# Kernel optimization log

Measured on AMD Instinct MI355X. Metric: run time of the kernel, lower is better.

## Reference

```python
import jax, jax.numpy as jnp
import numpy as np

L = 512
Z_DIM = 128
C = 128
EPS = 1e-5


def _ln(x, g, b):
    m = jnp.mean(x, axis=-1, keepdims=True)
    v = jnp.var(x, axis=-1, keepdims=True)
    return (x - m) * jax.lax.rsqrt(v + EPS) * g + b


def setup_inputs() -> dict:
    key = jax.random.key(0)
    ks = jax.random.split(key, 12)
    s_z = 1.0 / np.sqrt(Z_DIM)
    s_c = 1.0 / np.sqrt(C)
    return {
        "z": jax.random.normal(ks[0], (L, L, Z_DIM), dtype=jnp.float32),
        "norm_g": jnp.ones((Z_DIM,), jnp.float32),
        "norm_b": jnp.zeros((Z_DIM,), jnp.float32),
        "a_w": jax.random.normal(ks[1], (C, Z_DIM), jnp.float32) * s_z,
        "a_b": jnp.zeros((C,), jnp.float32),
        "ag_w": jax.random.normal(ks[2], (C, Z_DIM), jnp.float32) * s_z,
        "ag_b": jnp.zeros((C,), jnp.float32),
        "onorm_g": jnp.ones((C,), jnp.float32),
        "onorm_b": jnp.zeros((C,), jnp.float32),
        "o_w": jax.random.normal(ks[3], (Z_DIM, C), jnp.float32) * s_c,
        "o_b": jnp.zeros((Z_DIM,), jnp.float32),
        "g_w": jax.random.normal(ks[4], (Z_DIM, Z_DIM), jnp.float32) * s_z,
        "g_b": jnp.zeros((Z_DIM,), jnp.float32),
    }


def reference(z, norm_g, norm_b, a_w, a_b, ag_w, ag_b, onorm_g, onorm_b, o_w, o_b, g_w, g_b):
    zn = _ln(z, norm_g, norm_b)                                   # [L, L, z_dim]
    # gated projection; source computes b identically to a (alinear/aglinear for both)
    a = (zn @ a_w.T + a_b) * jax.nn.sigmoid(zn @ ag_w.T + ag_b)   # [L, L, c]
    o = jnp.einsum('ilc,jlc->ijc', a, a)                          # [L, L, c]
    o = _ln(o, onorm_g, onorm_b)
    o = o @ o_w.T + o_b                                           # [L, L, z_dim]
    return o * jax.nn.sigmoid(zn @ g_w.T + g_b)
```

## Files before the change

### kernel.cpp

```cpp
#include <hip/hip_runtime.h>
#include <stdint.h>

typedef unsigned short bf16;
typedef __attribute__((ext_vector_type(8))) short short8;
typedef __attribute__((ext_vector_type(4))) float f32x4;

#define MFMA16(a, b, c) __builtin_amdgcn_mfma_f32_16x16x32_bf16((a), (b), (c), 0, 0, 0)

__device__ __forceinline__ bf16 f2bf(float f) {
    unsigned u = __float_as_uint(f);
    u += 0x7fffu + ((u >> 16) & 1u);
    return (bf16)(u >> 16);
}
__device__ __forceinline__ float bf2f(bf16 s) { return __uint_as_float(((unsigned)s) << 16); }

__device__ __forceinline__ void gload_lds16(const void* g, void* lds) {
    auto gp = (const __attribute__((address_space(1))) unsigned int*)(uintptr_t)g;
    auto lp = (__attribute__((address_space(3))) unsigned int*)(uintptr_t)lds;
    __builtin_amdgcn_global_load_lds(gp, lp, 16, 0, 0);
}

__global__ __launch_bounds__(256) void k_wconv(const float* __restrict__ aw,
                                               const float* __restrict__ agw,
                                               const float* __restrict__ gw,
                                               const float* __restrict__ ow,
                                               bf16* __restrict__ wpk,
                                               bf16* __restrict__ owbf) {
    int i = blockIdx.x * 256 + threadIdx.x;
    if (i < 49152) {
        int m = i >> 14, r = i & 16383;
        int kk = r >> 12, rr = r & 4095;
        int nt = rr >> 9, li = rr & 511;
        int lane = li >> 3, e = li & 7;
        int lr = lane & 15, quad = lane >> 4;
        const float* s = (m == 0) ? aw : (m == 1) ? agw : gw;
        wpk[i] = f2bf(s[(nt * 16 + lr) * 128 + kk * 32 + quad * 8 + e]);
    } else {
        int k = i - 49152;
        owbf[k] = f2bf(ow[k]);
    }
}

__global__ __launch_bounds__(256) void k_ln_proj(const float* __restrict__ z,
                                                 const float* __restrict__ ng,
                                                 const float* __restrict__ nb,
                                                 const float* __restrict__ ab,
                                                 const float* __restrict__ agb,
                                                 const float* __restrict__ gbv,
                                                 const bf16* __restrict__ wpk,
                                                 bf16* __restrict__ a_t,
                                                 bf16* __restrict__ gbuf) {
    __shared__ bf16 zn_s[64 * 136];
    __shared__ bf16 st[8192];
    __shared__ float ng_s[128], nb_s[128];

    const int t = threadIdx.x;
    const int r0 = blockIdx.x * 64;

    if (t < 128) { ng_s[t] = ng[t]; nb_s[t] = nb[t]; }

    {
        int row = t >> 2, q = t & 3;
        const float* zp = z + (size_t)(r0 + row) * 128 + q * 32;
        float x[32];
        float s = 0.f, ss = 0.f;
#pragma unroll
        for (int i = 0; i < 8; ++i) {
            float4 v = ((const float4*)zp)[i];
            x[4 * i + 0] = v.x; x[4 * i + 1] = v.y; x[4 * i + 2] = v.z; x[4 * i + 3] = v.w;
        }
#pragma unroll
        for (int i = 0; i < 32; ++i) { s += x[i]; ss += x[i] * x[i]; }
        s += __shfl_xor(s, 1); ss += __shfl_xor(ss, 1);
        s += __shfl_xor(s, 2); ss += __shfl_xor(ss, 2);
        float mean = s * (1.f / 128.f);
        float var = ss * (1.f / 128.f) - mean * mean;
        float rstd = rsqrtf(var + 1e-5f);
        __syncthreads();
#pragma unroll
        for (int i = 0; i < 32; ++i) {
            int c = q * 32 + i;
            zn_s[row * 136 + c] = f2bf((x[i] - mean) * rstd * ng_s[c] + nb_s[c]);
        }
    }
    __syncthreads();

    const int lane = t & 63, w = t >> 6;
    const int lr = lane & 15, quad = lane >> 4;
    const int arow = w * 16 + lr;

    const short8* w0 = (const short8*)wpk + lane;
    const short8* w1 = (const short8*)(wpk + 16384) + lane;
    const short8* w2 = (const short8*)(wpk + 32768) + lane;

    f32x4 zero4 = {0.f, 0.f, 0.f, 0.f};
    f32x4 acc_a[8], acc_b[8];
#pragma unroll
    for (int nt = 0; nt < 8; ++nt) { acc_a[nt] = zero4; acc_b[nt] = zero4; }

#pragma unroll
    for (int kk = 0; kk < 4; ++kk) {
        short8 af = *(const short8*)&zn_s[arow * 136 + kk * 32 + quad * 8];
#pragma unroll
        for (int nt = 0; nt < 8; ++nt) {
            acc_a[nt] = MFMA16(af, w0[(kk * 8 + nt) * 64], acc_a[nt]);
            acc_b[nt] = MFMA16(af, w1[(kk * 8 + nt) * 64], acc_b[nt]);
        }
    }

#pragma unroll
    for (int nt = 0; nt < 8; ++nt) {
        int c = nt * 16 + lr;
        float abv = ab[c], agbv = agb[c];
#pragma unroll
        for (int r = 0; r < 4; ++r) {
            int row = w * 16 + quad * 4 + r;
            float av = acc_a[nt][r] + abv;
            float agvv = acc_b[nt][r] + agbv;
            st[c * 64 + row] = f2bf(av * (1.f / (1.f + __expf(-agvv))));
        }
    }
    __syncthreads();

#pragma unroll
    for (int i = 0; i < 4; ++i) {
        int idx = t + i * 256;
        int c = idx >> 3, part = idx & 7;
        *(uint4*)(a_t + (size_t)c * 262144 + r0 + part * 8) = *(const uint4*)&st[c * 64 + part * 8];
    }

#pragma unroll
    for (int nt = 0; nt < 8; ++nt) acc_a[nt] = zero4;
#pragma unroll
    for (int kk = 0; kk < 4; ++kk) {
        short8 af = *(const short8*)&zn_s[arow * 136 + kk * 32 + quad * 8];
#pragma unroll
        for (int nt = 0; nt < 8; ++nt)
            acc_a[nt] = MFMA16(af, w2[(kk * 8 + nt) * 64], acc_a[nt]);
    }
    __syncthreads();

#pragma unroll
    for (int nt = 0; nt < 8; ++nt) {
        int c = nt * 16 + lr;
        float gb0 = gbv[c];
#pragma unroll
        for (int r = 0; r < 4; ++r) {
            int row = w * 16 + quad * 4 + r;
            float v = acc_a[nt][r] + gb0;
            st[row * 128 + c] = f2bf(1.f / (1.f + __expf(-v)));
        }
    }
    __syncthreads();

#pragma unroll
    for (int i = 0; i < 4; ++i) {
        int idx = t + i * 256;
        int row = idx >> 4, part = idx & 15;
        *(uint4*)(gbuf + (size_t)(r0 + row) * 128 + part * 8) = *(const uint4*)&st[row * 128 + part * 8];
    }
}

__global__ __launch_bounds__(256) void k_einsum(const bf16* __restrict__ a_t,
                                                bf16* __restrict__ o_t) {
    __shared__ bf16 smem[16384];
    bf16* As = smem;
    bf16* Bs = smem + 8192;

    const int t = threadIdx.x;
    const int bx = blockIdx.x;
    const int c = bx >> 4;
    const int ti = (bx >> 2) & 3, tj = bx & 3;
    const int i0 = ti * 128, j0 = tj * 128;
    const size_t cbase = (size_t)c * 262144;
    const bf16* Ac = a_t + cbase;

    const int lane = t & 63, w = t >> 6;
    const int lr = lane & 15, quad = lane >> 4;
    const int wi = w >> 1, wj = w & 1;

    f32x4 zero4 = {0.f, 0.f, 0.f, 0.f};
    f32x4 acc[4][4];
#pragma unroll
    for (int mt = 0; mt < 4; ++mt)
#pragma unroll
        for (int nt = 0; nt < 4; ++nt) acc[mt][nt] = zero4;

    for (int kb = 0; kb < 8; ++kb) {
        __syncthreads();
#pragma unroll
        for (int q = 0; q < 4; ++q) {
            int t16 = (w << 8) + (q << 6) + lane;
            int row = t16 >> 3;
            int cb = t16 & 7;
            int cbg = cb ^ (row & 7);
            int gcol = kb * 64 + cbg * 8;
            gload_lds16(Ac + (size_t)(i0 + row) * 512 + gcol, As + (((w << 8) + (q << 6)) << 3));
            gload_lds16(Ac + (size_t)(j0 + row) * 512 + gcol, Bs + (((w << 8) + (q << 6)) << 3));
        }
        __syncthreads();
#pragma unroll
        for (int kk8 = 0; kk8 < 8; kk8 += 4) {
            short8 af[4], bfr[4];
#pragma unroll
            for (int mt = 0; mt < 4; ++mt) {
                int r = wi * 64 + mt * 16 + lr;
                af[mt] = *(const short8*)&As[r * 64 + (((kk8 + quad) ^ (lr & 7)) << 3)];
            }
#pragma unroll
            for (int nt = 0; nt < 4; ++nt) {
                int r = wj * 64 + nt * 16 + lr;
                bfr[nt] = *(const short8*)&Bs[r * 64 + (((kk8 + quad) ^ (lr & 7)) << 3)];
            }
#pragma unroll
            for (int mt = 0; mt < 4; ++mt)
#pragma unroll
                for (int nt = 0; nt < 4; ++nt)
                    acc[mt][nt] = MFMA16(af[mt], bfr[nt], acc[mt][nt]);
        }
    }

    __syncthreads();
    bf16* Cs = smem;
#pragma unroll
    for (int mt = 0; mt < 4; ++mt)
#pragma unroll
        for (int nt = 0; nt < 4; ++nt)
#pragma unroll
            for (int r = 0; r < 4; ++r) {
                int il = wi * 64 + mt * 16 + quad * 4 + r;
                int jl = wj * 64 + nt * 16 + lr;
                Cs[il * 128 + jl] = f2bf(acc[mt][nt][r]);
            }
    __syncthreads();
    bf16* Oc = o_t + cbase;
#pragma unroll
    for (int i = 0; i < 8; ++i) {
        int idx = t + (i << 8);
        int row = idx >> 4, part = idx & 15;
        *(uint4*)(Oc + (size_t)(i0 + row) * 512 + j0 + part * 8) = *(const uint4*)&Cs[row * 128 + part * 8];
    }
}

__global__ __launch_bounds__(256) void k_out(const bf16* __restrict__ o_t,
                                             const bf16* __restrict__ gbuf,
                                             const float* __restrict__ og,
                                             const float* __restrict__ ob,
                                             const bf16* __restrict__ owbf,
                                             const float* __restrict__ obias,
                                             float* __restrict__ out) {
    __shared__ bf16 pool[128 * 136];
    __shared__ float og_s[128], ob_s[128], obi_s[128];
    bf16* ot_s = pool;
    bf16* n_s = pool;

    const int t = threadIdx.x;
    const int p0 = blockIdx.x * 128;
    if (t < 128) { og_s[t] = og[t]; ob_s[t] = ob[t]; obi_s[t] = obias[t]; }

#pragma unroll
    for (int i = 0; i < 8; ++i) {
        int idx = t + (i << 8);
        int c = idx >> 4, part = idx & 15;
        *(uint4*)&ot_s[c * 128 + part * 8] = *(const uint4*)(o_t + (size_t)c * 262144 + p0 + part * 8);
    }
    __syncthreads();

    {
        int col = t >> 1, h = t & 1;
        float s = 0.f, ss = 0.f;
        float xv[64];
#pragma unroll
        for (int k = 0; k < 64; ++k) {
            float x = bf2f(ot_s[(h * 64 + k) * 128 + col]);
            xv[k] = x; s += x; ss += x * x;
        }
        s += __shfl_xor(s, 1); ss += __shfl_xor(ss, 1);
        float mean = s * (1.f / 128.f);
        float var = ss * (1.f / 128.f) - mean * mean;
        float rstd = rsqrtf(var + 1e-5f);
        __syncthreads();
#pragma unroll
        for (int k = 0; k < 64; ++k) {
            int cc = h * 64 + k;
            n_s[col * 136 + cc] = f2bf((xv[k] - mean) * rstd * og_s[cc] + ob_s[cc]);
        }
    }
    __syncthreads();

    const int lane = t & 63, w = t >> 6;
    const int lr = lane & 15, quad = lane >> 4;
    f32x4 zero4 = {0.f, 0.f, 0.f, 0.f};
    f32x4 acc[2][8];
#pragma unroll
    for (int mt = 0; mt < 2; ++mt)
#pragma unroll
        for (int nt = 0; nt < 8; ++nt) acc[mt][nt] = zero4;

#pragma unroll
    for (int kk = 0; kk < 4; ++kk) {
        short8 af[2];
#pragma unroll
        for (int mt = 0; mt < 2; ++mt)
            af[mt] = *(const short8*)&n_s[(w * 32 + mt * 16 + lr) * 136 + kk * 32 + quad * 8];
#pragma unroll
        for (int nt = 0; nt < 8; ++nt) {
            short8 bfr = *(const short8*)(owbf + (nt * 16 + lr) * 128 + kk * 32 + quad * 8);
            acc[0][nt] = MFMA16(af[0], bfr, acc[0][nt]);
            acc[1][nt] = MFMA16(af[1], bfr, acc[1][nt]);
        }
    }

#pragma unroll
    for (int mt = 0; mt < 2; ++mt)
#pragma unroll
        for (int nt = 0; nt < 8; ++nt) {
            int zd = nt * 16 + lr;
            float bias = obi_s[zd];
#pragma unroll
            for (int r = 0; r < 4; ++r) {
                int m = w * 32 + mt * 16 + quad * 4 + r;
                size_t off = (size_t)(p0 + m) * 128 + zd;
                out[off] = (acc[mt][nt][r] + bias) * bf2f(gbuf[off]);
            }
        }
}

extern "C" void kernel_launch(void* const* d_in, const int* in_sizes, int n_in,
                              void* d_out, int out_size, void* d_ws, size_t ws_size,
                              hipStream_t stream) {
    (void)in_sizes; (void)n_in; (void)out_size; (void)ws_size;
    const float* z   = (const float*)d_in[0];
    const float* ng  = (const float*)d_in[1];
    const float* nb  = (const float*)d_in[2];
    const float* aw  = (const float*)d_in[3];
    const float* ab  = (const float*)d_in[4];
    const float* agw = (const float*)d_in[5];
    const float* agb = (const float*)d_in[6];
    const float* ong = (const float*)d_in[7];
    const float* onb = (const float*)d_in[8];
    const float* ow  = (const float*)d_in[9];
    const float* obi = (const float*)d_in[10];
    const float* gw  = (const float*)d_in[11];
    const float* gbb = (const float*)d_in[12];

    char* ws = (char*)d_ws;
    bf16* wpk  = (bf16*)(ws);
    bf16* owbf = (bf16*)(ws + 98304);
    bf16* a_t  = (bf16*)(ws + 131072);
    bf16* gbuf = (bf16*)(ws + 131072 + 67108864);
    bf16* o_t  = (bf16*)(ws + 131072 + 2 * 67108864);

    k_wconv<<<256, 256, 0, stream>>>(aw, agw, gw, ow, wpk, owbf);
    k_ln_proj<<<4096, 256, 0, stream>>>(z, ng, nb, ab, agb, gbb, wpk, a_t, gbuf);
    k_einsum<<<2048, 256, 0, stream>>>(a_t, o_t);
    k_out<<<2048, 256, 0, stream>>>(o_t, gbuf, ong, onb, owbf, obi, (float*)d_out);
}
```

Before: 433.8 us.

## Stage projection weights in LDS via async global-to-LDS loads in LN-proj kernel

The LN+projection kernel now copies each of the three packed weight matrices into shared memory with global_load_lds, overlapping the first copy with the LayerNorm load, instead of reading MFMA B-fragments straight from global memory. All three GEMMs finish before the epilogue, which writes padded, vectorised transposed tiles into the reused weight and zn buffers. The goal is to cut repeated global and L2 weight traffic per block. In exchange it adds several block barriers, serialises weight staging between GEMMs, and keeps three accumulator sets live, which raises register pressure.

```diff
diff --git a/kernel.cpp b/kernel.cpp
--- a/kernel.cpp
+++ b/kernel.cpp
@@ -3,6 +3,7 @@
 
 typedef unsigned short bf16;
 typedef __attribute__((ext_vector_type(8))) short short8;
+typedef __attribute__((ext_vector_type(4))) unsigned short u16x4;
 typedef __attribute__((ext_vector_type(4))) float f32x4;
 
 #define MFMA16(a, b, c) __builtin_amdgcn_mfma_f32_16x16x32_bf16((a), (b), (c), 0, 0, 0)
@@ -51,11 +52,19 @@
                                                  bf16* __restrict__ a_t,
                                                  bf16* __restrict__ gbuf) {
     __shared__ bf16 zn_s[64 * 136];
-    __shared__ bf16 st[8192];
+    __shared__ bf16 w_s[16384];
     __shared__ float ng_s[128], nb_s[128];
 
     const int t = threadIdx.x;
     const int r0 = blockIdx.x * 64;
+
+    auto stage_w = [&](int mat) {
+#pragma unroll
+        for (int i = 0; i < 8; ++i) {
+            int idx = t + i * 256;
+            gload_lds16(wpk + mat * 16384 + idx * 8, w_s + idx * 8);
+        }
+    };
 
     if (t < 128) { ng_s[t] = ng[t]; nb_s[t] = nb[t]; }
 
@@ -63,12 +72,13 @@
         int row = t >> 2, q = t & 3;
         const float* zp = z + (size_t)(r0 + row) * 128 + q * 32;
         float x[32];
-        float s = 0.f, ss = 0.f;
 #pragma unroll
         for (int i = 0; i < 8; ++i) {
             float4 v = ((const float4*)zp)[i];
             x[4 * i + 0] = v.x; x[4 * i + 1] = v.y; x[4 * i + 2] = v.z; x[4 * i + 3] = v.w;
         }
+        stage_w(0);
+        float s = 0.f, ss = 0.f;
 #pragma unroll
         for (int i = 0; i < 32; ++i) { s += x[i]; ss += x[i] * x[i]; }
         s += __shfl_xor(s, 1); ss += __shfl_xor(ss, 1);
@@ -89,35 +99,63 @@
     const int lr = lane & 15, quad = lane >> 4;
     const int arow = w * 16 + lr;
 
-    const short8* w0 = (const short8*)wpk + lane;
-    const short8* w1 = (const short8*)(wpk + 16384) + lane;
-    const short8* w2 = (const short8*)(wpk + 32768) + lane;
+    auto gemmv = [&](f32x4* acc) {
+        const short8* ws8 = (const short8*)w_s;
+#pragma unroll
+        for (int kk = 0; kk < 4; ++kk) {
+            short8 af = *(const short8*)&zn_s[arow * 136 + kk * 32 + quad * 8];
+#pragma unroll
+            for (int nt = 0; nt < 8; ++nt)
+                acc[nt] = MFMA16(af, ws8[(kk * 8 + nt) * 64 + lane], acc[nt]);
+        }
+    };
 
     f32x4 zero4 = {0.f, 0.f, 0.f, 0.f};
-    f32x4 acc_a[8], acc_b[8];
-#pragma unroll
-    for (int nt = 0; nt < 8; ++nt) { acc_a[nt] = zero4; acc_b[nt] = zero4; }
-
-#pragma unroll
-    for (int kk = 0; kk < 4; ++kk) {
-        short8 af = *(const short8*)&zn_s[arow * 136 + kk * 32 + quad * 8];
+    f32x4 acc_a[8], acc_b[8], acc_g[8];
+#pragma unroll
+    for (int nt = 0; nt < 8; ++nt) { acc_a[nt] = zero4; acc_b[nt] = zero4; acc_g[nt] = zero4; }
+
+    gemmv(acc_a);
+    __syncthreads();
+    stage_w(1);
+    __syncthreads();
+    gemmv(acc_b);
+    __syncthreads();
+    stage_w(2);
+    __syncthreads();
+    gemmv(acc_g);
+    __syncthreads();
+
+    bf16* st_a = w_s;
+    bf16* st_g = zn_s;
+
+    {
+        const int row0 = w * 16 + quad * 4;
 #pragma unroll
         for (int nt = 0; nt < 8; ++nt) {
-            acc_a[nt] = MFMA16(af, w0[(kk * 8 + nt) * 64], acc_a[nt]);
-            acc_b[nt] = MFMA16(af, w1[(kk * 8 + nt) * 64], acc_b[nt]);
-        }
-    }
-
-#pragma unroll
-    for (int nt = 0; nt < 8; ++nt) {
-        int c = nt * 16 + lr;
-        float abv = ab[c], agbv = agb[c];
-#pragma unroll
-        for (int r = 0; r < 4; ++r) {
-            int row = w * 16 + quad * 4 + r;
-            float av = acc_a[nt][r] + abv;
-            float agvv = acc_b[nt][r] + agbv;
-            st[c * 64 + row] = f2bf(av * (1.f / (1.f + __expf(-agvv))));
+            int c = nt * 16 + lr;
+            float abv = ab[c], agbv = agb[c];
+            u16x4 pk;
+#pragma unroll
+            for (int r = 0; r < 4; ++r) {
+                float av = acc_a[nt][r] + abv;
+                float agvv = acc_b[nt][r] + agbv;
+                pk[r] = f2bf(av * (1.f / (1.f + __expf(-agvv))));
+            }
+            *(u16x4*)&st_a[c * 72 + row0] = pk;
+        }
+    }
+    {
+#pragma unroll
+        for (int nt = 0; nt < 8; ++nt) {
+            int c = nt * 16 + lr;
+            float gb0 = gbv[c];
+#pragma unroll
+            for (int r = 0; r < 4; ++r) {
+                int row = w * 16 + quad * 4 + r;
+                float v = acc_g[nt][r] + gb0;
+                st_g[row * 136 + c] = f2bf(1.f / (1.f + __expf(-v)));
+            }
         }
     }
     __syncthreads();
@@ -126,38 +164,13 @@
     for (int i = 0; i < 4; ++i) {
         int idx = t + i * 256;
         int c = idx >> 3, part = idx & 7;
-        *(uint4*)(a_t + (size_t)c * 262144 + r0 + part * 8) = *(const uint4*)&st[c * 64 + part * 8];
-    }
-
-#pragma unroll
-    for (int nt = 0; nt < 8; ++nt) acc_a[nt] = zero4;
-#pragma unroll
-    for (int kk = 0; kk < 4; ++kk) {
-        short8 af = *(const short8*)&zn_s[arow * 136 + kk * 32 + quad * 8];
-#pragma unroll
-        for (int nt = 0; nt < 8; ++nt)
-            acc_a[nt] = MFMA16(af, w2[(kk * 8 + nt) * 64], acc_a[nt]);
-    }
-    __syncthreads();
-
-#pragma unroll
-    for (int nt = 0; nt < 8; ++nt) {
-        int c = nt * 16 + lr;
-        float gb0 = gbv[c];
-#pragma unroll
-        for (int r = 0; r < 4; ++r) {
-            int row = w * 16 + quad * 4 + r;
-            float v = acc_a[nt][r] + gb0;
-            st[row * 128 + c] = f2bf(1.f / (1.f + __expf(-v)));
-        }
-    }
-    __syncthreads();
-
+        *(uint4*)(a_t + (size_t)c * 262144 + r0 + part * 8) = *(const uint4*)&st_a[c * 72 + part * 8];
+    }
 #pragma unroll
     for (int i = 0; i < 4; ++i) {
         int idx = t + i * 256;
         int row = idx >> 4, part = idx & 15;
-        *(uint4*)(gbuf + (size_t)(r0 + row) * 128 + part * 8) = *(const uint4*)&st[row * 128 + part * 8];
+        *(uint4*)(gbuf + (size_t)(r0 + row) * 128 + part * 8) = *(const uint4*)&st_g[row * 136 + part * 8];
     }
 }
 
```

Result: no change. 429.9 us (-0.9%).
